# Kernel optimization log

Hardware: AMD Instinct MI355X
Metric: run time of the kernel (lower is better)

Reference implementation:

```python
import jax, jax.numpy as jnp
import numpy as np

K = 3        # kernel_size
STRIDE = 1
PAD = 1
DIL = 1


def conv2d(x, w, b, stride, pad):
    y = jax.lax.conv_general_dilated(
        x, w, window_strides=(stride, stride),
        padding=[(pad, pad), (pad, pad)],
        dimension_numbers=('NCHW', 'OIHW', 'NCHW'))
    return y + b[None, :, None, None]


def bilinear_sample(x_t, py, px):
    """x_t: [B,H,W,C]; py,px: [B,Ho,Wo] float sample coords. Zero padding outside."""
    B, H, W, C = x_t.shape
    b = jnp.arange(B)[:, None, None]
    y0 = jnp.floor(py)
    x0 = jnp.floor(px)
    wy = py - y0
    wx = px - x0
    out = jnp.zeros(py.shape + (C,), x_t.dtype)
    for dy, dx, wgt in ((0, 0, (1 - wy) * (1 - wx)),
                        (0, 1, (1 - wy) * wx),
                        (1, 0, wy * (1 - wx)),
                        (1, 1, wy * wx)):
        yy = y0 + dy
        xx = x0 + dx
        valid = (yy >= 0) & (yy < H) & (xx >= 0) & (xx < W)
        yi = jnp.clip(yy, 0, H - 1).astype(jnp.int32)
        xi = jnp.clip(xx, 0, W - 1).astype(jnp.int32)
        g = x_t[b, yi, xi]                      # [B,Ho,Wo,C] gather
        out = out + g * (wgt * valid)[..., None]
    return out


def deform_conv2d(x, offset, weight, bias):
    """torchvision-style deform_conv2d (v1, 1 offset group).
    x: [B,C,H,W]; offset: [B,2*K*K,Ho,Wo] with (dy,dx) interleaved per tap;
    weight: [O,C,K,K]; bias: [O]."""
    B, C, H, W = x.shape
    O = weight.shape[0]
    Ho, Wo = offset.shape[2], offset.shape[3]
    x_t = jnp.transpose(x, (0, 2, 3, 1))        # [B,H,W,C]
    off = offset.reshape(B, K * K, 2, Ho, Wo)   # [B,K2,(dy,dx),Ho,Wo]
    base_y = (jnp.arange(Ho) * STRIDE - PAD).astype(x.dtype)
    base_x = (jnp.arange(Wo) * STRIDE - PAD).astype(x.dtype)
    samples = []
    for k in range(K * K):                      # fixed 9-tap loop
        ki, kj = divmod(k, K)
        py = base_y[None, :, None] + ki * DIL + off[:, k, 0]   # [B,Ho,Wo]
        px = base_x[None, None, :] + kj * DIL + off[:, k, 1]
        samples.append(bilinear_sample(x_t, py, px))
    sampled = jnp.stack(samples)                # [K2,B,Ho,Wo,C]
    out = jnp.einsum('kbhwc,ock->bohw', sampled, weight.reshape(O, C, K * K))
    return out + bias[None, :, None, None]


def setup_inputs() -> dict:
    key = jax.random.key(0)
    k0, k1, k2, k3 = jax.random.split(key, 4)
    B, Cin, Cout, H, W = 8, 64, 64, 128, 128
    x = jax.random.normal(k0, (B, Cin, H, W), jnp.float32)
    # offset conv: small init so sampled offsets stay near the regular grid
    w_off = jax.random.normal(k1, (2 * K * K, Cin, K, K), jnp.float32) * 0.01
    b_off = jnp.zeros((2 * K * K,), jnp.float32)
    w = jax.random.normal(k2, (Cout, Cin, K, K), jnp.float32) * (1.0 / np.sqrt(Cin * K * K))
    b = jax.random.normal(k3, (Cout,), jnp.float32) * 0.01
    return {"x": x, "w_off": w_off, "b_off": b_off, "w": w, "b": b}


def reference(x, w_off, b_off, w, b):
    offset = conv2d(x, w_off, b_off, STRIDE, PAD)   # [B,18,Ho,Wo]
    return deform_conv2d(x, offset, w, b)           # [B,64,Ho,Wo]
```

## Files before the change

### kernel.cpp

```cpp
#include <hip/hip_runtime.h>

#define B_   8
#define C_   64
#define O_   64
#define H_   128
#define W_   128
#define HO_  128
#define WO_  128
#define K2_  9
#define MOFF 18
#define PLANE (H_*W_)
#define KTOT 576

#define BROWS 6
#define BCOLS 132
#define PSTRIDE (BROWS*BCOLS*8)

typedef short bf16x8 __attribute__((ext_vector_type(8)));
typedef float f32x16 __attribute__((ext_vector_type(16)));
typedef float f32x2  __attribute__((ext_vector_type(2)));
typedef unsigned int u32x4 __attribute__((ext_vector_type(4)));

__device__ __forceinline__ unsigned short f2bf(float f) {
    unsigned u = __float_as_uint(f);
    u += 0x7fff + ((u >> 16) & 1);
    return (unsigned short)(u >> 16);
}
__device__ __forceinline__ float bf2f(short v) {
    return __uint_as_float(((unsigned)(unsigned short)v) << 16);
}
__device__ __forceinline__ f32x2 unpk(unsigned w) {
    f32x2 r;
    r.x = __uint_as_float(w << 16);
    r.y = __uint_as_float(w & 0xffff0000u);
    return r;
}

__global__ __launch_bounds__(256) void prep_kernel(const float* __restrict__ x,
                                                   const float* __restrict__ w,
                                                   const float* __restrict__ w_off,
                                                   unsigned short* __restrict__ xt,
                                                   unsigned short* __restrict__ wbf) {
    __shared__ __align__(16) unsigned short T[64 * 132];
    const int tid = threadIdx.x;
    if (blockIdx.x >= B_ * H_) {
        int i = (blockIdx.x - B_ * H_) * 256 + tid;
        if (i < 96 * KTOT) {
            int o = i / KTOT, pos = i % KTOT;
            int cc = pos / 144, r = pos % 144, t = r / 16, cl = r % 16;
            int c = cc * 16 + cl;
            unsigned short v;
            if (o < O_)             v = f2bf(w[o * KTOT + c * 9 + t]);
            else if (o < O_ + MOFF) v = f2bf(w_off[(o - O_) * KTOT + c * 9 + t]);
            else                    v = 0;
            wbf[i] = v;
        }
        return;
    }
    const int b = blockIdx.x & 7;
    const int y = blockIdx.x >> 3;
    const float4* src4 = (const float4*)(x + (size_t)b * C_ * PLANE + y * W_);
    for (int i = tid; i < 64 * 32; i += 256) {
        int c = i >> 5, px4 = i & 31;
        float4 v = src4[c * (PLANE / 4) + px4];
        ushort4 t = { f2bf(v.x), f2bf(v.y), f2bf(v.z), f2bf(v.w) };
        *(ushort4*)&T[c * 132 + px4 * 4] = t;
    }
    __syncthreads();
    for (int j = tid; j < 128 * 4; j += 256) {
        int cc = j >> 7, px = j & 127;
        unsigned short* dst = xt + ((size_t)(cc * B_ + b) * PLANE + y * W_ + px) * 16;
        ushort4 v0 = { T[(cc*16+ 0)*132+px], T[(cc*16+ 1)*132+px],
                       T[(cc*16+ 2)*132+px], T[(cc*16+ 3)*132+px] };
        ushort4 v1 = { T[(cc*16+ 4)*132+px], T[(cc*16+ 5)*132+px],
                       T[(cc*16+ 6)*132+px], T[(cc*16+ 7)*132+px] };
        ushort4 v2 = { T[(cc*16+ 8)*132+px], T[(cc*16+ 9)*132+px],
                       T[(cc*16+10)*132+px], T[(cc*16+11)*132+px] };
        ushort4 v3 = { T[(cc*16+12)*132+px], T[(cc*16+13)*132+px],
                       T[(cc*16+14)*132+px], T[(cc*16+15)*132+px] };
        *(ushort4*)(dst)      = v0;
        *(ushort4*)(dst + 4)  = v1;
        *(ushort4*)(dst + 8)  = v2;
        *(ushort4*)(dst + 12) = v3;
    }
}

__global__ __launch_bounds__(512, 4) void fused_kernel(const unsigned short* __restrict__ xt,
        const unsigned short* __restrict__ wobf, const float* __restrict__ b_off,
        const unsigned short* __restrict__ wbf, const float* __restrict__ bias,
        float* __restrict__ out) {
    __shared__ __align__(16) unsigned short band[2 * PSTRIDE];
    __shared__ float lo[MOFF * 256];
    const int tid  = threadIdx.x;
    const int id   = blockIdx.x;
    const int b    = id & 7;
    const int r0   = (id >> 3) << 1;
    const int wv   = tid >> 6;
    const int rl   = wv >> 2;
    const int ho   = r0 + rl;
    const int lane = tid & 63;
    const int m    = lane & 31;
    const int kh   = lane >> 5;
    const int pxg  = ((wv & 3) << 5) + m;

    auto stage = [&](const unsigned short* xtc, int ybase, int nrows) {
        const int npos = nrows * BCOLS;
        uint4 va[2], vb[2];
        #pragma unroll
        for (int it = 0; it < 2; ++it) {
            va[it] = (uint4){0, 0, 0, 0};
            vb[it] = (uint4){0, 0, 0, 0};
            int j = tid + it * 512;
            if (j < npos) {
                int r = j / BCOLS, c = j - r * BCOLS;
                int y = ybase + r, x = c - 2;
                if (((unsigned)y < (unsigned)H_) && ((unsigned)x < (unsigned)W_)) {
                    const uint4* gp = (const uint4*)(xtc + (y * W_ + x) * 16);
                    va[it] = gp[0];
                    vb[it] = gp[1];
                }
            }
        }
        #pragma unroll
        for (int it = 0; it < 2; ++it) {
            int j = tid + it * 512;
            if (j < npos) {
                int r = j / BCOLS, c = j - r * BCOLS;
                int s = (r * BCOLS + c) * 8;
                *(uint4*)&band[s]           = va[it];
                *(uint4*)&band[PSTRIDE + s] = vb[it];
            }
        }
    };

    f32x16 acc0 = {};
    for (int cc = 0; cc < 4; ++cc) {
        const unsigned short* xtc = xt + (size_t)(cc * B_ + b) * PLANE * 16;
        stage(xtc, r0 - 1, 4);
        __syncthreads();
        #pragma unroll
        for (int ks = 0; ks < 9; ++ks) {
            bf16x8 a = *(const bf16x8*)&wobf[m * KTOT + cc * 144 + ks * 16 + kh * 8];
            bf16x8 s = *(const bf16x8*)&band[kh * PSTRIDE +
                        ((rl + ks / 3) * BCOLS + pxg + ks % 3 + 1) * 8];
            acc0 = __builtin_amdgcn_mfma_f32_32x32x16_bf16(a, s, acc0, 0, 0, 0);
        }
        __syncthreads();
    }
    #pragma unroll
    for (int r = 0; r < 16; ++r) {
        int mo = (r & 3) + ((r >> 2) << 3) + (kh << 2);
        if (mo < MOFF) lo[mo * 256 + rl * 128 + pxg] = acc0[r] + b_off[mo];
    }
    __syncthreads();

    f32x16 acc[2] = {};
    for (int cc = 0; cc < 4; ++cc) {
        const unsigned short* xtc = xt + (size_t)(cc * B_ + b) * PLANE * 16;
        stage(xtc, r0 - 2, 6);
        __syncthreads();
        #pragma unroll
        for (int ks = 0; ks < 9; ++ks) {
            float py  = (float)(ho - 1 + ks / 3) + lo[(2 * ks) * 256 + rl * 128 + pxg];
            float pxc = (float)(pxg - 1 + ks % 3) + lo[(2 * ks + 1) * 256 + rl * 128 + pxg];
            float fy = floorf(py), fx = floorf(pxc);
            float wy = py - fy,    wx = pxc - fx;
            int y0 = (int)fy, x0 = (int)fx;
            int rb_ = y0 - r0 + 2, cb = x0 + 2;
            bool oob = ((unsigned)rb_ > 4u) || ((unsigned)cb > 130u);
            int rbc = min(max(rb_, 0), 4), cbc = min(max(cb, 0), 130);
            const unsigned short* bp = &band[kh * PSTRIDE + (rbc * BCOLS + cbc) * 8];
            const uint4 c00 = *(const uint4*)bp;
            const uint4 c01 = *(const uint4*)(bp + 8);
            const uint4 c10 = *(const uint4*)(bp + BCOLS * 8);
            const uint4 c11 = *(const uint4*)(bp + BCOLS * 8 + 8);
            const f32x2 wx2 = { wx, wx };
            const f32x2 wy2 = { wy, wy };
            u32x4 vr;
            #pragma unroll
            for (int pq = 0; pq < 4; ++pq) {
                unsigned w00 = (pq==0)?c00.x:(pq==1)?c00.y:(pq==2)?c00.z:c00.w;
                unsigned w01 = (pq==0)?c01.x:(pq==1)?c01.y:(pq==2)?c01.z:c01.w;
                unsigned w10 = (pq==0)?c10.x:(pq==1)?c10.y:(pq==2)?c10.z:c10.w;
                unsigned w11 = (pq==0)?c11.x:(pq==1)?c11.y:(pq==2)?c11.z:c11.w;
                f32x2 a2 = unpk(w00), b2 = unpk(w01);
                f32x2 c2 = unpk(w10), d2 = unpk(w11);
                f32x2 top = a2 + wx2 * (b2 - a2);
                f32x2 bot = c2 + wx2 * (d2 - c2);
                f32x2 r2  = top + wy2 * (bot - top);
                unsigned pk;
                asm("v_cvt_pk_bf16_f32 %0, %1, %2" : "=v"(pk) : "v"(r2.x), "v"(r2.y));
                vr[pq] = pk;
            }
            bf16x8 v = __builtin_bit_cast(bf16x8, vr);
            if (__builtin_expect(__any(oob), 0)) {
                if (oob) {
                    float s8[8];
                    #pragma unroll
                    for (int j = 0; j < 8; ++j) s8[j] = 0.f;
                    #pragma unroll
                    for (int c2i = 0; c2i < 4; ++c2i) {
                        int yy = y0 + (c2i >> 1);
                        int xx = x0 + (c2i & 1);
                        bool valid = ((unsigned)yy < (unsigned)H_) && ((unsigned)xx < (unsigned)W_);
                        int yc = min(max(yy, 0), H_ - 1);
                        int xc = min(max(xx, 0), W_ - 1);
                        float wgt = ((c2i >> 1) ? wy : 1.f - wy) * ((c2i & 1) ? wx : 1.f - wx);
                        wgt = valid ? wgt : 0.f;
                        const unsigned short* rp = xtc + (yc * W_ + xc) * 16 + kh * 8;
                        bf16x8 u = *(const bf16x8*)rp;
                        #pragma unroll
                        for (int j = 0; j < 8; ++j) s8[j] += wgt * bf2f(u[j]);
                    }
                    #pragma unroll
                    for (int j = 0; j < 8; ++j) v[j] = (short)f2bf(s8[j]);
                }
            }
            bf16x8 a0 = *(const bf16x8*)&wbf[m * KTOT + cc * 144 + ks * 16 + kh * 8];
            bf16x8 a1 = *(const bf16x8*)&wbf[(32 + m) * KTOT + cc * 144 + ks * 16 + kh * 8];
            acc[0] = __builtin_amdgcn_mfma_f32_32x32x16_bf16(a0, v, acc[0], 0, 0, 0);
            acc[1] = __builtin_amdgcn_mfma_f32_32x32x16_bf16(a1, v, acc[1], 0, 0, 0);
        }
        __syncthreads();
    }

    {
        float* op = out + (size_t)b * O_ * PLANE + ho * WO_ + pxg;
        #pragma unroll
        for (int nt = 0; nt < 2; ++nt) {
            #pragma unroll
            for (int r = 0; r < 16; ++r) {
                int mo = (nt << 5) + (r & 3) + ((r >> 2) << 3) + (kh << 2);
                __builtin_nontemporal_store(acc[nt][r] + bias[mo], op + (size_t)mo * PLANE);
            }
        }
    }
}

extern "C" void kernel_launch(void* const* d_in, const int* in_sizes, int n_in,
                              void* d_out, int out_size, void* d_ws, size_t ws_size,
                              hipStream_t stream) {
    const float* x     = (const float*)d_in[0];
    const float* w_off = (const float*)d_in[1];
    const float* b_off = (const float*)d_in[2];
    const float* w     = (const float*)d_in[3];
    const float* bias  = (const float*)d_in[4];
    float* out = (float*)d_out;

    unsigned short* wbf  = (unsigned short*)d_ws;
    unsigned short* wobf = wbf + O_ * KTOT;
    unsigned short* xt   = wobf + 32 * KTOT;

    const int wblocks = (96 * KTOT + 255) / 256;
    prep_kernel <<<B_ * H_ + wblocks, 256, 0, stream>>>(x, w, w_off, xt, wbf);
    fused_kernel<<<B_ * HO_ / 2, 512, 0, stream>>>(xt, wobf, b_off, wbf, bias, out);
}
```

Baseline: 144.6 us.

## Assign one output row per block and split output channels across wave halves

Each block now handles one output row instead of two. The 8 waves split the 64 output channels in halves, so each wave issues one MFMA per tap instead of two and the block count doubles. The staged band shrinks to 5 rows and the offset buffer to one row, which raises the launch-bounds occupancy hint to 6. In exchange, each wave recomputes the bilinear sampling for its half of the channels, so that work is duplicated. Halo rows are also restaged per row rather than shared across two rows, and only half the waves do the offset conv.

```diff
diff --git a/kernel.cpp b/kernel.cpp
--- a/kernel.cpp
+++ b/kernel.cpp
@@ -12,7 +12,7 @@
 #define PLANE (H_*W_)
 #define KTOT 576
 
-#define BROWS 6
+#define BROWS 5
 #define BCOLS 132
 #define PSTRIDE (BROWS*BCOLS*8)
 
@@ -85,25 +85,24 @@
     }
 }
 
-__global__ __launch_bounds__(512, 4) void fused_kernel(const unsigned short* __restrict__ xt,
+__global__ __launch_bounds__(512, 6) void fused_kernel(const unsigned short* __restrict__ xt,
         const unsigned short* __restrict__ wobf, const float* __restrict__ b_off,
         const unsigned short* __restrict__ wbf, const float* __restrict__ bias,
         float* __restrict__ out) {
     __shared__ __align__(16) unsigned short band[2 * PSTRIDE];
-    __shared__ float lo[MOFF * 256];
+    __shared__ float lo[MOFF * 128];
     const int tid  = threadIdx.x;
     const int id   = blockIdx.x;
     const int b    = id & 7;
-    const int r0   = (id >> 3) << 1;
+    const int ho   = id >> 3;
     const int wv   = tid >> 6;
-    const int rl   = wv >> 2;
-    const int ho   = r0 + rl;
+    const int mh   = wv >> 2;
     const int lane = tid & 63;
     const int m    = lane & 31;
     const int kh   = lane >> 5;
     const int pxg  = ((wv & 3) << 5) + m;
 
-    auto stage = [&](const unsigned short* xtc, int ybase, int nrows) {
+    auto stage = [&](const unsigned short* xtc, int r0, int nrows) {
         const int npos = nrows * BCOLS;
         uint4 va[2], vb[2];
         #pragma unroll
@@ -113,7 +112,7 @@
             int j = tid + it * 512;
             if (j < npos) {
                 int r = j / BCOLS, c = j - r * BCOLS;
-                int y = ybase + r, x = c - 2;
+                int y = ho - 2 + r0 + r, x = c - 2;
                 if (((unsigned)y < (unsigned)H_) && ((unsigned)x < (unsigned)W_)) {
                     const uint4* gp = (const uint4*)(xtc + (y * W_ + x) * 16);
                     va[it] = gp[0];
@@ -126,49 +125,55 @@
             int j = tid + it * 512;
             if (j < npos) {
                 int r = j / BCOLS, c = j - r * BCOLS;
-                int s = (r * BCOLS + c) * 8;
+                int s = ((r0 + r) * BCOLS + c) * 8;
                 *(uint4*)&band[s]           = va[it];
                 *(uint4*)&band[PSTRIDE + s] = vb[it];
             }
         }
     };
 
-    f32x16 acc0 = {};
+    {
+        f32x16 acc0 = {};
+        for (int cc = 0; cc < 4; ++cc) {
+            const unsigned short* xtc = xt + (size_t)(cc * B_ + b) * PLANE * 16;
+            stage(xtc, 1, 3);
+            __syncthreads();
+            if (mh == 0) {
+                #pragma unroll
+                for (int ks = 0; ks < 9; ++ks) {
+                    bf16x8 a = *(const bf16x8*)&wobf[m * KTOT + cc * 144 + ks * 16 + kh * 8];
+                    bf16x8 s = *(const bf16x8*)&band[kh * PSTRIDE +
+                                ((1 + ks / 3) * BCOLS + pxg + ks % 3 + 1) * 8];
+                    acc0 = __builtin_amdgcn_mfma_f32_32x32x16_bf16(a, s, acc0, 0, 0, 0);
+                }
+            }
+            __syncthreads();
+        }
+        if (mh == 0) {
+            #pragma unroll
+            for (int r = 0; r < 16; ++r) {
+                int mo = (r & 3) + ((r >> 2) << 3) + (kh << 2);
+                if (mo < MOFF) lo[mo * 128 + pxg] = acc0[r] + b_off[mo];
+            }
+        }
+    }
+    __syncthreads();
+
+    f32x16 acc = {};
     for (int cc = 0; cc < 4; ++cc) {
         const unsigned short* xtc = xt + (size_t)(cc * B_ + b) * PLANE * 16;
-        stage(xtc, r0 - 1, 4);
+        stage(xtc, 0, 5);
         __syncthreads();
         #pragma unroll
         for (int ks = 0; ks < 9; ++ks) {
-            bf16x8 a = *(const bf16x8*)&wobf[m * KTOT + cc * 144 + ks * 16 + kh * 8];
-            bf16x8 s = *(const bf16x8*)&band[kh * PSTRIDE +
-                        ((rl + ks / 3) * BCOLS + pxg + ks % 3 + 1) * 8];
-            acc0 = __builtin_amdgcn_mfma_f32_32x32x16_bf16(a, s, acc0, 0, 0, 0);
-        }
-        __syncthreads();
-    }
-    #pragma unroll
-    for (int r = 0; r < 16; ++r) {
-        int mo = (r & 3) + ((r >> 2) << 3) + (kh << 2);
-        if (mo < MOFF) lo[mo * 256 + rl * 128 + pxg] = acc0[r] + b_off[mo];
-    }
-    __syncthreads();
-
-    f32x16 acc[2] = {};
-    for (int cc = 0; cc < 4; ++cc) {
-        const unsigned short* xtc = xt + (size_t)(cc * B_ + b) * PLANE * 16;
-        stage(xtc, r0 - 2, 6);
-        __syncthreads();
-        #pragma unroll
-        for (int ks = 0; ks < 9; ++ks) {
-            float py  = (float)(ho - 1 + ks / 3) + lo[(2 * ks) * 256 + rl * 128 + pxg];
-            float pxc = (float)(pxg - 1 + ks % 3) + lo[(2 * ks + 1) * 256 + rl * 128 + pxg];
+            float py  = (float)(ho - 1 + ks / 3) + lo[(2 * ks) * 128 + pxg];
+            float pxc = (float)(pxg - 1 + ks % 3) + lo[(2 * ks + 1) * 128 + pxg];
             float fy = floorf(py), fx = floorf(pxc);
             float wy = py - fy,    wx = pxc - fx;
             int y0 = (int)fy, x0 = (int)fx;
-            int rb_ = y0 - r0 + 2, cb = x0 + 2;
-            bool oob = ((unsigned)rb_ > 4u) || ((unsigned)cb > 130u);
-            int rbc = min(max(rb_, 0), 4), cbc = min(max(cb, 0), 130);
+            int rb_ = y0 - ho + 2, cb = x0 + 2;
+            bool oob = ((unsigned)rb_ > 3u) || ((unsigned)cb > 130u);
+            int rbc = min(max(rb_, 0), 3), cbc = min(max(cb, 0), 130);
             const unsigned short* bp = &band[kh * PSTRIDE + (rbc * BCOLS + cbc) * 8];
             const uint4 c00 = *(const uint4*)bp;
             const uint4 c01 = *(const uint4*)(bp + 8);
@@ -216,10 +221,8 @@
                     for (int j = 0; j < 8; ++j) v[j] = (short)f2bf(s8[j]);
                 }
             }
-            bf16x8 a0 = *(const bf16x8*)&wbf[m * KTOT + cc * 144 + ks * 16 + kh * 8];
-            bf16x8 a1 = *(const bf16x8*)&wbf[(32 + m) * KTOT + cc * 144 + ks * 16 + kh * 8];
-            acc[0] = __builtin_amdgcn_mfma_f32_32x32x16_bf16(a0, v, acc[0], 0, 0, 0);
-            acc[1] = __builtin_amdgcn_mfma_f32_32x32x16_bf16(a1, v, acc[1], 0, 0, 0);
+            bf16x8 a0 = *(const bf16x8*)&wbf[(mh * 32 + m) * KTOT + cc * 144 + ks * 16 + kh * 8];
+            acc = __builtin_amdgcn_mfma_f32_32x32x16_bf16(a0, v, acc, 0, 0, 0);
         }
         __syncthreads();
     }
@@ -227,12 +230,9 @@
     {
         float* op = out + (size_t)b * O_ * PLANE + ho * WO_ + pxg;
         #pragma unroll
-        for (int nt = 0; nt < 2; ++nt) {
-            #pragma unroll
-            for (int r = 0; r < 16; ++r) {
-                int mo = (nt << 5) + (r & 3) + ((r >> 2) << 3) + (kh << 2);
-                __builtin_nontemporal_store(acc[nt][r] + bias[mo], op + (size_t)mo * PLANE);
-            }
+        for (int r = 0; r < 16; ++r) {
+            int mo = (mh << 5) + (r & 3) + ((r >> 2) << 3) + (kh << 2);
+            __builtin_nontemporal_store(acc[r] + bias[mo], op + (size_t)mo * PLANE);
         }
     }
 }
@@ -253,5 +253,5 @@
 
     const int wblocks = (96 * KTOT + 255) / 256;
     prep_kernel <<<B_ * H_ + wblocks, 256, 0, stream>>>(x, w, w_off, xt, wbf);
-    fused_kernel<<<B_ * HO_ / 2, 512, 0, stream>>>(xt, wobf, b_off, wbf, bias, out);
-}
+    fused_kernel<<<B_ * HO_, 512, 0, stream>>>(xt, wobf, b_off, wbf, bias, out);
+}
```

New measurement: 161.1 us. +11.5%, slower.
